# Performance work log

Hardware: AMD Instinct MI355X
Metric: run time of the kernel (lower is better)

## Reference

```python
import jax, jax.numpy as jnp
import numpy as np

EPS = 1e-6

def layer_norm(x, g, b):
    mu = jnp.mean(x, axis=-1, keepdims=True)
    var = jnp.mean((x - mu) ** 2, axis=-1, keepdims=True)
    return g * (x - mu) / jnp.sqrt(var + EPS) + b

def linear_mha(v_in, k_in, q_in, wq, bq, wk, bk, wv, bv, wo, bo, num_heads, d_model):
    b, s, _ = q_in.shape
    dv = d_model // num_heads
    q = q_in @ wq + bq                       # [b, s, h] (depth-1 per head)
    k = k_in @ wk + bk                       # [b, s, h]
    v = (v_in @ wv + bv).reshape(b, s, num_heads, dv).transpose(0, 2, 1, 3)  # [b,h,s,dv]
    q = q.transpose(0, 2, 1)                 # [b, h, s]
    k = k.transpose(0, 2, 1)                 # [b, h, s]
    # phi(k)^T v collapses seq: rank-1 per head -> [b, h, dv]
    kv = jnp.einsum('bhs,bhsd->bhd', jax.nn.sigmoid(k), v)
    # NOTE: tf.cumsum(axis=1) on shape (b, h, 1, dv) cumsums over the HEAD axis
    s_cum = jnp.cumsum(kv, axis=1)           # [b, h, dv]
    out = jnp.einsum('bhs,bhd->bhsd', jax.nn.sigmoid(q), s_cum)  # [b,h,s,dv]
    out = out.transpose(0, 2, 1, 3).reshape(b, s, d_model)
    return out @ wo + bo

def setup_inputs() -> dict:
    key = jax.random.key(0)
    ks = jax.random.split(key, 24)
    B, S, D, H, F = 4, 4096, 1024, 16, 4096
    gl = lambda k, shp: jax.random.uniform(k, shp, jnp.float32,
        -jnp.sqrt(6.0 / (shp[0] + shp[1])), jnp.sqrt(6.0 / (shp[0] + shp[1])))
    inp = {
        'x': jax.random.normal(ks[0], (B, S, D), jnp.float32),
        'enc': jax.random.normal(ks[1], (B, S, D), jnp.float32),
        'wq1': gl(ks[2], (D, H)), 'bq1': jnp.zeros((H,), jnp.float32),
        'wk1': gl(ks[3], (D, H)), 'bk1': jnp.zeros((H,), jnp.float32),
        'wv1': gl(ks[4], (D, D)), 'bv1': jnp.zeros((D,), jnp.float32),
        'wo1': gl(ks[5], (D, D)), 'bo1': jnp.zeros((D,), jnp.float32),
        'wq2': gl(ks[6], (D, H)), 'bq2': jnp.zeros((H,), jnp.float32),
        'wk2': gl(ks[7], (D, H)), 'bk2': jnp.zeros((H,), jnp.float32),
        'wv2': gl(ks[8], (D, D)), 'bv2': jnp.zeros((D,), jnp.float32),
        'wo2': gl(ks[9], (D, D)), 'bo2': jnp.zeros((D,), jnp.float32),
        'wf1': gl(ks[10], (D, F)), 'bf1': jnp.zeros((F,), jnp.float32),
        'wf2': gl(ks[11], (F, D)), 'bf2': jnp.zeros((D,), jnp.float32),
        'g1': jnp.ones((D,), jnp.float32), 'be1': jnp.zeros((D,), jnp.float32),
        'g2': jnp.ones((D,), jnp.float32), 'be2': jnp.zeros((D,), jnp.float32),
        'g3': jnp.ones((D,), jnp.float32), 'be3': jnp.zeros((D,), jnp.float32),
    }
    return inp

def reference(x, enc, wq1, bq1, wk1, bk1, wv1, bv1, wo1, bo1,
              wq2, bq2, wk2, bk2, wv2, bv2, wo2, bo2,
              wf1, bf1, wf2, bf2, g1, be1, g2, be2, g3, be3):
    H, D = 16, x.shape[-1]
    attn1 = linear_mha(x, x, x, wq1, bq1, wk1, bk1, wv1, bv1, wo1, bo1, H, D)
    out1 = layer_norm(attn1 + x, g1, be1)
    attn2 = linear_mha(enc, enc, out1, wq2, bq2, wk2, bk2, wv2, bv2, wo2, bo2, H, D)
    out2 = layer_norm(attn2 + out1, g2, be2)
    ffn = jax.nn.relu(out2 @ wf1 + bf1) @ wf2 + bf2
    out3 = layer_norm(ffn + out2, g3, be3)
    return (out3, jnp.zeros_like(out3), jnp.zeros_like(out3))
```

## Files before the change

### kernel.cpp

```cpp
#include <hip/hip_runtime.h>
#include <cstdint>

typedef unsigned short u16;
typedef __bf16 bf16x8 __attribute__((ext_vector_type(8)));
typedef float f32x4 __attribute__((ext_vector_type(4)));

__device__ __forceinline__ float bf2f(u16 h) {
  union { uint32_t u; float f; } v; v.u = (uint32_t)h << 16; return v.f;
}
__device__ __forceinline__ u16 f2bf(float f) {
  union { float f; uint32_t u; } v; v.f = f;
  uint32_t r = v.u + 0x7fffu + ((v.u >> 16) & 1u);
  return (u16)(r >> 16);
}
__device__ __forceinline__ float sigmoidf_(float x) {
  return 1.0f / (1.0f + __expf(-x));
}
__device__ __forceinline__ void load_lds16(const void* g, void* l) {
  __builtin_amdgcn_global_load_lds(
      (const __attribute__((address_space(1))) void*)g,
      (__attribute__((address_space(3))) void*)l, 16, 0, 0);
}
__device__ __forceinline__ bf16x8 cvt8(const float* p) {
  float4 a = *(const float4*)p, b = *(const float4*)(p + 4);
  union { u16 u[8]; bf16x8 v; } r;
  r.u[0] = f2bf(a.x); r.u[1] = f2bf(a.y); r.u[2] = f2bf(a.z); r.u[3] = f2bf(a.w);
  r.u[4] = f2bf(b.x); r.u[5] = f2bf(b.y); r.u[6] = f2bf(b.z); r.u[7] = f2bf(b.w);
  return r.v;
}
#define BAR() __builtin_amdgcn_s_barrier()

__global__ __launch_bounds__(256) void transpose_cvt(
    const float* __restrict__ in, u16* __restrict__ out, int K, int N) {
  __shared__ float t[32][33];
  int n0 = blockIdx.x * 32, k0 = blockIdx.y * 32;
  int tx = threadIdx.x & 31, ty = threadIdx.x >> 5;
#pragma unroll
  for (int i = 0; i < 32; i += 8)
    t[ty + i][tx] = in[(long)(k0 + ty + i) * N + n0 + tx];
  __syncthreads();
#pragma unroll
  for (int i = 0; i < 32; i += 8)
    out[(long)(n0 + ty + i) * K + k0 + tx] = f2bf(t[tx][ty + i]);
}

template <int QBF>
__global__ __launch_bounds__(256) void proj_mfma(
    const void* __restrict__ xq_, const float* __restrict__ xk,
    const float* __restrict__ wq, const float* __restrict__ bq,
    const float* __restrict__ wk, const float* __restrict__ bk,
    float* __restrict__ qout, float* __restrict__ kout) {
  __shared__ __attribute__((aligned(16))) u16 wt[2][16384];
  __shared__ __attribute__((aligned(16))) float red[4][64][8];
  const int tid = threadIdx.x;
  for (int kq = 0; kq < 4; kq++) {
    int k = kq * 256 + tid;
    const float4* q4 = (const float4*)(wq + (long)k * 16);
    const float4* k4 = (const float4*)(wk + (long)k * 16);
#pragma unroll
    for (int p = 0; p < 4; p++) {
      float4 qv = q4[p], kv = k4[p];
      float qf[4] = {qv.x, qv.y, qv.z, qv.w};
      float kf[4] = {kv.x, kv.y, kv.z, kv.w};
#pragma unroll
      for (int j = 0; j < 4; j++) {
        int c = p * 4 + j;
        int off = (c * 2048 + k * 2) ^ ((c & 7) << 4);
        *(u16*)((char*)wt[0] + off) = f2bf(qf[j]);
        *(u16*)((char*)wt[1] + off) = f2bf(kf[j]);
      }
    }
  }
  __syncthreads();
  const int wv = tid >> 6, lane = tid & 63;
  const int lrow = lane & 15, g = lane >> 4;
  const long tok0 = (long)blockIdx.x * 16;
  const long arow = (tok0 + lrow) * 1024 + wv * 256 + g * 8;
  const int swz = (lrow & 7) << 4;
  const int wbase = lrow * 2048 + wv * 512 + g * 16;
  f32x4 accq = {}, acck = {};
#pragma unroll
  for (int mf = 0; mf < 8; mf++) {
    bf16x8 aq_;
    if (QBF)
      aq_ = *(const bf16x8*)((const u16*)xq_ + arow + mf * 32);
    else
      aq_ = cvt8((const float*)xq_ + arow + mf * 32);
    bf16x8 ak_ = cvt8(xk + arow + mf * 32);
    int off = (wbase + mf * 64) ^ swz;
    bf16x8 bq_ = *(const bf16x8*)((const char*)wt[0] + off);
    bf16x8 bk_ = *(const bf16x8*)((const char*)wt[1] + off);
    accq = __builtin_amdgcn_mfma_f32_16x16x32_bf16(aq_, bq_, accq, 0, 0, 0);
    acck = __builtin_amdgcn_mfma_f32_16x16x32_bf16(ak_, bk_, acck, 0, 0, 0);
  }
  *(f32x4*)&red[wv][lane][0] = accq;
  *(f32x4*)&red[wv][lane][4] = acck;
  __syncthreads();
  if (tid < 64) {
    f32x4 q0 = *(const f32x4*)&red[0][tid][0];
    f32x4 k0 = *(const f32x4*)&red[0][tid][4];
#pragma unroll
    for (int w = 1; w < 4; w++) {
      q0 += *(const f32x4*)&red[w][tid][0];
      k0 += *(const f32x4*)&red[w][tid][4];
    }
    int col = tid & 15, r0 = (tid >> 4) * 4;
    float bqv = bq[col], bkv = bk[col];
#pragma unroll
    for (int i = 0; i < 4; i++) {
      qout[(tok0 + r0 + i) * 16 + col] = q0[i] + bqv;
      kout[(tok0 + r0 + i) * 16 + col] = k0[i] + bkv;
    }
  }
}

__global__ __launch_bounds__(256) void ksum(const float* __restrict__ kp,
                                            const float* __restrict__ x,
                                            float* __restrict__ ypart,
                                            float* __restrict__ spart) {
  __shared__ __attribute__((aligned(16))) float sk[256][20];
  __shared__ float ssl[16][17];
  const int tid = threadIdx.x;
  const int cc = blockIdx.x, sc = blockIdx.y, b = blockIdx.z;
  const int cl = tid & 63, sg = tid >> 6;
  const int col0 = cc * 128 + cl;
  float acc0[16], acc1[16];
#pragma unroll
  for (int h = 0; h < 16; h++) { acc0[h] = 0.f; acc1[h] = 0.f; }
  float ss = 0.f;
  for (int tile = 0; tile < 2; tile++) {
    const int s0 = sc * 512 + tile * 256;
    const float* kr = kp + ((long)b * 4096 + s0 + tid) * 16;
#pragma unroll
    for (int p = 0; p < 4; p++) {
      float4 k4 = *(const float4*)(kr + p * 4);
      *(float4*)&sk[tid][p * 4] = make_float4(
          sigmoidf_(k4.x), sigmoidf_(k4.y), sigmoidf_(k4.z), sigmoidf_(k4.w));
    }
    __syncthreads();
    {
      int g2 = tid >> 4, h2 = tid & 15;
      float s_ = 0.f;
#pragma unroll
      for (int i = 0; i < 16; i++) s_ += sk[g2 * 16 + i][h2];
      ssl[g2][h2] = s_;
    }
    __syncthreads();
    if (tid < 16) {
      float s_ = 0.f;
#pragma unroll
      for (int gg = 0; gg < 16; gg++) s_ += ssl[gg][tid];
      ss += s_;
    }
    const float* xr = x + ((long)b * 4096 + s0 + sg * 64) * 1024 + col0;
    for (int j = 0; j < 64; j++) {
      float xv0 = xr[(long)j * 1024];
      float xv1 = xr[(long)j * 1024 + 64];
      const float4* skr = (const float4*)sk[sg * 64 + j];
#pragma unroll
      for (int p = 0; p < 4; p++) {
        float4 s4 = skr[p];
        acc0[p * 4 + 0] += s4.x * xv0; acc1[p * 4 + 0] += s4.x * xv1;
        acc0[p * 4 + 1] += s4.y * xv0; acc1[p * 4 + 1] += s4.y * xv1;
        acc0[p * 4 + 2] += s4.z * xv0; acc1[p * 4 + 2] += s4.z * xv1;
        acc0[p * 4 + 3] += s4.w * xv0; acc1[p * 4 + 3] += s4.w * xv1;
      }
    }
    __syncthreads();
  }
  long pbase = (long)(b * 32 + sc * 4 + sg) * 16384 + col0;
#pragma unroll
  for (int h = 0; h < 16; h++) {
    ypart[pbase + h * 1024] = acc0[h];
    ypart[pbase + h * 1024 + 64] = acc1[h];
  }
  if (tid < 16) spart[(b * 8 + sc) * 16 + tid] = ss;
}

__global__ __launch_bounds__(256) void kv_small(
    const float* __restrict__ ypart, const float* __restrict__ spart,
    const float* __restrict__ wvw, const float* __restrict__ bv,
    float* __restrict__ kv) {
  __shared__ float yl[1024];
  __shared__ float red[4][64];
  const int tid = threadIdx.x;
  const int b = blockIdx.x >> 4, h = blockIdx.x & 15;
  for (int c = tid; c < 1024; c += 256) {
    float s_ = 0.f;
    const float* yp = ypart + (long)(b * 32) * 16384 + h * 1024 + c;
#pragma unroll
    for (int p = 0; p < 32; p++) s_ += yp[(long)p * 16384];
    yl[c] = s_;
  }
  __syncthreads();
  const int wv_ = tid >> 6, d = tid & 63;
  float acc = 0.f;
  const float* wcol = wvw + h * 64 + d;
  for (int c = wv_ * 256; c < wv_ * 256 + 256; c++)
    acc += yl[c] * wcol[(long)c * 1024];
  red[wv_][d] = acc;
  __syncthreads();
  if (tid < 64) {
    float ss = 0.f;
#pragma unroll
    for (int s_ = 0; s_ < 8; s_++) ss += spart[(b * 8 + s_) * 16 + h];
    kv[(b * 16 + h) * 64 + tid] = red[0][tid] + red[1][tid] + red[2][tid] +
                                  red[3][tid] + ss * bv[h * 64 + tid];
  }
}

__global__ __launch_bounds__(256) void zker(const float* __restrict__ kvb,
                                            const float* __restrict__ wo,
                                            float* __restrict__ z) {
  __shared__ float sc_[64];
  const int tid = threadIdx.x;
  const int b = blockIdx.x >> 4, h = blockIdx.x & 15;
  if (tid < 64) {
    float run = 0.f;
    for (int hh = 0; hh <= h; hh++) run += kvb[(b * 16 + hh) * 64 + tid];
    sc_[tid] = run;
  }
  __syncthreads();
  float4 acc = make_float4(0.f, 0.f, 0.f, 0.f);
  for (int d = 0; d < 64; d++) {
    float s_ = sc_[d];
    float4 w = ((const float4*)(wo + (long)(h * 64 + d) * 1024))[tid];
    acc.x += s_ * w.x; acc.y += s_ * w.y;
    acc.z += s_ * w.z; acc.w += s_ * w.w;
  }
  ((float4*)(z + (long)(b * 16 + h) * 1024))[tid] = acc;
}

template <int OMODE>
__global__ __launch_bounds__(256) void ln_attn(
    const float* __restrict__ qp, const float* __restrict__ z,
    const float* __restrict__ bo, const float* __restrict__ r,
    const float* __restrict__ g, const float* __restrict__ be,
    float* __restrict__ outf, u16* __restrict__ outb) {
  __shared__ float zs[16][1024];
  __shared__ float sq16[16];
  __shared__ float s1[4], s2[4];
  const int tid = threadIdx.x;
  const int b = blockIdx.x >> 8;
  const float4* zg = (const float4*)(z + (long)b * 16384);
  float4* zl = (float4*)zs;
#pragma unroll
  for (int i = 0; i < 16; i++) zl[i * 256 + tid] = zg[i * 256 + tid];
  float4 gv = ((const float4*)g)[tid];
  float4 bev = ((const float4*)be)[tid];
  float4 bov = ((const float4*)bo)[tid];
  const int wid = tid >> 6, lane = tid & 63;
  for (int rr_ = 0; rr_ < 16; rr_++) {
    long row = (long)blockIdx.x * 16 + rr_;
    if (tid < 16) sq16[tid] = sigmoidf_(qp[row * 16 + tid]);
    __syncthreads();
    float4 rv = ((const float4*)(r + row * 1024))[tid];
    float y0 = bov.x + rv.x, y1 = bov.y + rv.y;
    float y2 = bov.z + rv.z, y3 = bov.w + rv.w;
#pragma unroll
    for (int h = 0; h < 16; h++) {
      float s_ = sq16[h];
      float4 zv = *(const float4*)&zs[h][tid * 4];
      y0 += s_ * zv.x; y1 += s_ * zv.y; y2 += s_ * zv.z; y3 += s_ * zv.w;
    }
    float s = y0 + y1 + y2 + y3;
    float q = y0 * y0 + y1 * y1 + y2 * y2 + y3 * y3;
#pragma unroll
    for (int o = 32; o > 0; o >>= 1) {
      s += __shfl_down(s, o);
      q += __shfl_down(q, o);
    }
    if (lane == 0) { s1[wid] = s; s2[wid] = q; }
    __syncthreads();
    s = s1[0] + s1[1] + s1[2] + s1[3];
    q = s2[0] + s2[1] + s2[2] + s2[3];
    float mu = s * (1.f / 1024.f);
    float var = q * (1.f / 1024.f) - mu * mu;
    float inv = rsqrtf(fmaxf(var, 0.f) + 1e-6f);
    float o0 = gv.x * (y0 - mu) * inv + bev.x;
    float o1 = gv.y * (y1 - mu) * inv + bev.y;
    float o2 = gv.z * (y2 - mu) * inv + bev.z;
    float o3 = gv.w * (y3 - mu) * inv + bev.w;
    ((float4*)(outf + row * 1024))[tid] = make_float4(o0, o1, o2, o3);
    if (OMODE == 2) {
      uint2 ob;
      ob.x = (uint32_t)f2bf(o0) | ((uint32_t)f2bf(o1) << 16);
      ob.y = (uint32_t)f2bf(o2) | ((uint32_t)f2bf(o3) << 16);
      ((uint2*)(outb + row * 1024))[tid] = ob;
    }
    __syncthreads();
  }
}

template <int ACT>
__global__ __launch_bounds__(512) void gemm256(
    const u16* __restrict__ A, const u16* __restrict__ BT,
    const float* __restrict__ bias, u16* __restrict__ C, int M, int N,
    int K) {
  __shared__ __attribute__((aligned(16))) u16 lds[65536];
  const int tid = threadIdx.x;
  const int wid = tid >> 6, lane = tid & 63;
  const int wm = wid >> 2, wn = wid & 3;
  const int lrow = lane & 15, g = lane >> 4;

  int nwg = gridDim.x * gridDim.y;
  int orig = blockIdx.y * gridDim.x + blockIdx.x;
  int wg = (nwg & 7) ? orig : ((orig & 7) * (nwg >> 3) + (orig >> 3));
  const long bn = (long)(wg % gridDim.x) * 256;
  const long bm = (long)(wg / gridDim.x) * 256;

  const int rr = wid * 16 + (lane >> 2);
  const int esrc = ((lane & 3) * 8) ^ (((lane >> 5) & 1) * 16);
  const u16* Abase = A + (bm + rr) * (long)K + esrc;
  const u16* Bbase = BT + (bn + rr) * (long)K + esrc;
  const long jstep = (long)128 * K;
  char* ldsc = (char*)lds;
  const int ldsw = wid * 1024;

  const int swr = ((lrow >> 3) & 1) * 32;
  const int aoff = (wm * 128 + lrow) * 64 + ((g * 16) ^ swr);
  const int boff = 32768 + (wn * 64 + lrow) * 64 + ((g * 16) ^ swr);

  f32x4 acc[8][4] = {};
  const int KT = K >> 6;

  auto stage2 = [&](int buf, int kk, int kt, int half) {
    int dA = buf * 65536 + kk * 16384 + ldsw;
    if (half == 0) {
      const u16* sA = Abase + (long)kt * 64 + kk * 32;
      load_lds16(sA, ldsc + dA);
      load_lds16(sA + jstep, ldsc + dA + 8192);
    } else {
      const u16* sB = Bbase + (long)kt * 64 + kk * 32;
      load_lds16(sB, ldsc + dA + 32768);
      load_lds16(sB + jstep, ldsc + dA + 40960);
    }
  };

#define LDAB8(BUF, KK)                                                      \
  {                                                                         \
    const char* _b = ldsc + (BUF) * 65536 + (KK) * 16384;                   \
    _Pragma("unroll") for (int m = 0; m < 4; m++)                           \
        af[m] = *(const bf16x8*)(_b + aoff + m * 1024);                     \
    _Pragma("unroll") for (int n = 0; n < 4; n++)                           \
        bq[n] = *(const bf16x8*)(_b + boff + n * 1024);                     \
  }
#define LDA4(BUF, KK)                                                       \
  {                                                                         \
    const char* _b = ldsc + (BUF) * 65536 + (KK) * 16384;                   \
    _Pragma("unroll") for (int m = 4; m < 8; m++)                           \
        af[m] = *(const bf16x8*)(_b + aoff + m * 1024);                     \
  }
#define MMA16(M0)                                                           \
  __builtin_amdgcn_s_setprio(1);                                            \
  _Pragma("unroll") for (int m = M0; m < M0 + 4; m++)                       \
  _Pragma("unroll") for (int n = 0; n < 4; n++)                             \
      acc[m][n] = __builtin_amdgcn_mfma_f32_16x16x32_bf16(af[m], bq[n],     \
                                                          acc[m][n], 0, 0,  \
                                                          0);               \
  __builtin_amdgcn_s_setprio(0);
#define WLG0() asm volatile("s_waitcnt lgkmcnt(0)" ::: "memory")
#define WVM4() asm volatile("s_waitcnt vmcnt(4)" ::: "memory")
#define WVM0() asm volatile("s_waitcnt vmcnt(0)" ::: "memory")

  bf16x8 af[8], bq[4];

  stage2(0, 0, 0, 0);
  stage2(0, 0, 0, 1);
  stage2(0, 1, 0, 0);
  stage2(0, 1, 0, 1);
  WVM4();
  BAR();

  for (int kt = 0; kt + 1 < KT; ++kt) {
    const int b0 = kt & 1, b1 = b0 ^ 1;
    LDAB8(b0, 0);
    stage2(b1, 0, kt + 1, 0);
    BAR(); WLG0();
    MMA16(0);
    BAR();
    LDA4(b0, 0);
    stage2(b1, 0, kt + 1, 1);
    WVM4();
    BAR(); WLG0();
    MMA16(4);
    BAR();
    LDAB8(b0, 1);
    stage2(b1, 1, kt + 1, 0);
    BAR(); WLG0();
    MMA16(0);
    BAR();
    LDA4(b0, 1);
    stage2(b1, 1, kt + 1, 1);
    WVM4();
    BAR(); WLG0();
    MMA16(4);
    BAR();
  }
  {
    const int b0 = (KT - 1) & 1;
    LDAB8(b0, 0);
    BAR(); WLG0();
    MMA16(0);
    BAR();
    LDA4(b0, 0);
    WVM0();
    BAR(); WLG0();
    MMA16(4);
    BAR();
    LDAB8(b0, 1);
    BAR(); WLG0();
    MMA16(0);
    BAR();
    LDA4(b0, 1);
    BAR(); WLG0();
    MMA16(4);
    BAR();
  }

#pragma unroll
  for (int n = 0; n < 4; n++) {
    int cl = wn * 64 + n * 16 + lrow;
    float bb = bias[bn + cl];
#pragma unroll
    for (int m = 0; m < 8; m++) {
      int rl = wm * 128 + m * 16 + g * 4;
#pragma unroll
      for (int i = 0; i < 4; i++) {
        float v = acc[m][n][i] + bb;
        if (ACT == 1) v = fmaxf(v, 0.f);
        lds[(rl + i) * 256 + cl] = f2bf(v);
      }
    }
  }
  BAR();
  const uint4* lv = (const uint4*)lds;
#pragma unroll
  for (int it = 0; it < 16; it++) {
    int idx = it * 512 + tid;
    int row = idx >> 5;
    int cu = (idx & 31) * 8;
    *(uint4*)&C[(bm + row) * (long)N + bn + cu] = lv[idx];
  }
#undef LDAB8
#undef LDA4
#undef MMA16
#undef WLG0
#undef WVM4
#undef WVM0
}

__global__ __launch_bounds__(256) void ln_res(const u16* __restrict__ a,
                                              const float* __restrict__ r,
                                              const float* __restrict__ g,
                                              const float* __restrict__ be,
                                              float* __restrict__ outf) {
  long row = blockIdx.x;
  int tid = threadIdx.x;
  uint2 av = ((const uint2*)(a + row * 1024))[tid];
  float4 rv = ((const float4*)(r + row * 1024))[tid];
  float y[4];
  y[0] = bf2f((u16)(av.x & 0xffff)) + rv.x;
  y[1] = bf2f((u16)(av.x >> 16)) + rv.y;
  y[2] = bf2f((u16)(av.y & 0xffff)) + rv.z;
  y[3] = bf2f((u16)(av.y >> 16)) + rv.w;
  float s = y[0] + y[1] + y[2] + y[3];
  float q = y[0] * y[0] + y[1] * y[1] + y[2] * y[2] + y[3] * y[3];
#pragma unroll
  for (int o = 32; o > 0; o >>= 1) {
    s += __shfl_down(s, o);
    q += __shfl_down(q, o);
  }
  __shared__ float s1[4], s2[4];
  int wid = tid >> 6, lane = tid & 63;
  if (lane == 0) { s1[wid] = s; s2[wid] = q; }
  __syncthreads();
  s = s1[0] + s1[1] + s1[2] + s1[3];
  q = s2[0] + s2[1] + s2[2] + s2[3];
  float mu = s * (1.f / 1024.f);
  float var = q * (1.f / 1024.f) - mu * mu;
  float inv = rsqrtf(fmaxf(var, 0.f) + 1e-6f);
  float4 gv = ((const float4*)g)[tid], bv = ((const float4*)be)[tid];
  float o0 = gv.x * (y[0] - mu) * inv + bv.x;
  float o1 = gv.y * (y[1] - mu) * inv + bv.y;
  float o2 = gv.z * (y[2] - mu) * inv + bv.z;
  float o3 = gv.w * (y[3] - mu) * inv + bv.w;
  ((float4*)(outf + row * 1024))[tid] = make_float4(o0, o1, o2, o3);
}

extern "C" void kernel_launch(void* const* d_in, const int* in_sizes, int n_in,
                              void* d_out, int out_size, void* d_ws,
                              size_t ws_size, hipStream_t stream) {
  const float* x   = (const float*)d_in[0];
  const float* enc = (const float*)d_in[1];
  const float* wq1 = (const float*)d_in[2];  const float* bq1 = (const float*)d_in[3];
  const float* wk1 = (const float*)d_in[4];  const float* bk1 = (const float*)d_in[5];
  const float* wv1 = (const float*)d_in[6];  const float* bv1 = (const float*)d_in[7];
  const float* wo1 = (const float*)d_in[8];  const float* bo1 = (const float*)d_in[9];
  const float* wq2 = (const float*)d_in[10]; const float* bq2 = (const float*)d_in[11];
  const float* wk2 = (const float*)d_in[12]; const float* bk2 = (const float*)d_in[13];
  const float* wv2 = (const float*)d_in[14]; const float* bv2 = (const float*)d_in[15];
  const float* wo2 = (const float*)d_in[16]; const float* bo2 = (const float*)d_in[17];
  const float* wf1 = (const float*)d_in[18]; const float* bf1 = (const float*)d_in[19];
  const float* wf2 = (const float*)d_in[20]; const float* bf2 = (const float*)d_in[21];
  const float* g1 = (const float*)d_in[22];  const float* be1 = (const float*)d_in[23];
  const float* g2 = (const float*)d_in[24];  const float* be2 = (const float*)d_in[25];
  const float* g3 = (const float*)d_in[26];  const float* be3 = (const float*)d_in[27];
  (void)in_sizes; (void)n_in; (void)out_size; (void)ws_size;

  const size_t S = (size_t)16384 * 1024;
  float* O0 = (float*)d_out;

  char* base = (char*)d_ws;
  size_t off = 0;
  auto alloc = [&](size_t bytes) -> void* {
    void* p = base + off;
    off += (bytes + 255) & ~(size_t)255;
    return p;
  };
  u16* WT1    = (u16*)alloc((size_t)4096 * 1024 * 2);
  u16* WT2    = (u16*)alloc((size_t)4096 * 1024 * 2);
  float* qb   = (float*)alloc((size_t)16384 * 16 * 4);
  float* kb   = (float*)alloc((size_t)16384 * 16 * 4);
  float* ypart= (float*)alloc((size_t)4 * 32 * 16 * 1024 * 4);
  float* spart= (float*)alloc((size_t)4 * 8 * 16 * 4);
  float* kvb  = (float*)alloc((size_t)4 * 16 * 64 * 4);
  float* zb   = (float*)alloc((size_t)4 * 16 * 1024 * 4);
  u16* FA     = (u16*)alloc(S * 2);
  u16* FM     = (u16*)alloc((size_t)16384 * 4096 * 2);
  u16* O1b    = (u16*)alloc(S * 2);
  u16* O2b    = (u16*)alloc(S * 2);
  float* O1f  = (float*)alloc(S * 4);
  float* O2f  = (float*)alloc(S * 4);

  const int T = 16384;
  dim3 blk(256), gblk(512);

  proj_mfma<0><<<1024, blk, 0, stream>>>(x, x, wq1, bq1, wk1, bk1, qb, kb);
  ksum<<<dim3(8, 8, 4), blk, 0, stream>>>(kb, x, ypart, spart);
  kv_small<<<64, blk, 0, stream>>>(ypart, spart, wv1, bv1, kvb);
  zker<<<64, blk, 0, stream>>>(kvb, wo1, zb);
  ln_attn<2><<<1024, blk, 0, stream>>>(qb, zb, bo1, x, g1, be1, O1f, O1b);

  proj_mfma<1><<<1024, blk, 0, stream>>>(O1b, enc, wq2, bq2, wk2, bk2, qb, kb);
  ksum<<<dim3(8, 8, 4), blk, 0, stream>>>(kb, enc, ypart, spart);
  kv_small<<<64, blk, 0, stream>>>(ypart, spart, wv2, bv2, kvb);
  zker<<<64, blk, 0, stream>>>(kvb, wo2, zb);
  ln_attn<2><<<1024, blk, 0, stream>>>(qb, zb, bo2, O1f, g2, be2, O2f, O2b);

  transpose_cvt<<<dim3(128, 32), blk, 0, stream>>>(wf1, WT1, 1024, 4096);
  transpose_cvt<<<dim3(32, 128), blk, 0, stream>>>(wf2, WT2, 4096, 1024);
  gemm256<1><<<dim3(16, 64), gblk, 0, stream>>>(O2b, WT1, bf1, FM, T, 4096, 1024);
  gemm256<0><<<dim3(4, 64), gblk, 0, stream>>>(FM, WT2, bf2, FA, T, 1024, 4096);
  ln_res<<<16384, blk, 0, stream>>>(FA, O2f, g3, be3, O0);

  hipMemsetAsync((float*)d_out + S, 0, 2 * S * 4, stream);
}
```

Before: 593.2 us.

## Give each wave its own token tile in q/k projection, drop LDS reduction

The q/k projection kernel now assigns each wave a full 16-token row tile over the whole K dimension instead of splitting K across four waves. This removes the LDS cross-wave reduction and its barrier, and cuts the grid from 1024 to 256 blocks, so each block's per-block conversion of the weights into LDS is amortised over four times as many tokens. For the first layer, where q and k share the same input, a SAME template flag reuses the converted A fragment instead of loading and converting x twice. The cost is fewer blocks (less parallelism) and a longer serial MFMA chain per wave.

```diff
diff --git a/kernel.cpp b/kernel.cpp
--- a/kernel.cpp
+++ b/kernel.cpp
@@ -44,14 +44,13 @@
     out[(long)(n0 + ty + i) * K + k0 + tx] = f2bf(t[tx][ty + i]);
 }
 
-template <int QBF>
+template <int SAME, int QBF>
 __global__ __launch_bounds__(256) void proj_mfma(
     const void* __restrict__ xq_, const float* __restrict__ xk,
     const float* __restrict__ wq, const float* __restrict__ bq,
     const float* __restrict__ wk, const float* __restrict__ bk,
     float* __restrict__ qout, float* __restrict__ kout) {
   __shared__ __attribute__((aligned(16))) u16 wt[2][16384];
-  __shared__ __attribute__((aligned(16))) float red[4][64][8];
   const int tid = threadIdx.x;
   for (int kq = 0; kq < 4; kq++) {
     int k = kq * 256 + tid;
@@ -74,43 +73,34 @@
   __syncthreads();
   const int wv = tid >> 6, lane = tid & 63;
   const int lrow = lane & 15, g = lane >> 4;
-  const long tok0 = (long)blockIdx.x * 16;
-  const long arow = (tok0 + lrow) * 1024 + wv * 256 + g * 8;
+  const long tok0 = (long)blockIdx.x * 64 + wv * 16;
   const int swz = (lrow & 7) << 4;
-  const int wbase = lrow * 2048 + wv * 512 + g * 16;
+  const long arow = (tok0 + lrow) * 1024 + g * 8;
   f32x4 accq = {}, acck = {};
-#pragma unroll
-  for (int mf = 0; mf < 8; mf++) {
+#pragma unroll 8
+  for (int ks = 0; ks < 32; ks++) {
     bf16x8 aq_;
     if (QBF)
-      aq_ = *(const bf16x8*)((const u16*)xq_ + arow + mf * 32);
+      aq_ = *(const bf16x8*)((const u16*)xq_ + arow + ks * 32);
     else
-      aq_ = cvt8((const float*)xq_ + arow + mf * 32);
-    bf16x8 ak_ = cvt8(xk + arow + mf * 32);
-    int off = (wbase + mf * 64) ^ swz;
+      aq_ = cvt8((const float*)xq_ + arow + ks * 32);
+    bf16x8 ak_;
+    if (SAME)
+      ak_ = aq_;
+    else
+      ak_ = cvt8(xk + arow + ks * 32);
+    int off = (lrow * 2048 + ks * 64 + g * 16) ^ swz;
     bf16x8 bq_ = *(const bf16x8*)((const char*)wt[0] + off);
     bf16x8 bk_ = *(const bf16x8*)((const char*)wt[1] + off);
     accq = __builtin_amdgcn_mfma_f32_16x16x32_bf16(aq_, bq_, accq, 0, 0, 0);
     acck = __builtin_amdgcn_mfma_f32_16x16x32_bf16(ak_, bk_, acck, 0, 0, 0);
   }
-  *(f32x4*)&red[wv][lane][0] = accq;
-  *(f32x4*)&red[wv][lane][4] = acck;
-  __syncthreads();
-  if (tid < 64) {
-    f32x4 q0 = *(const f32x4*)&red[0][tid][0];
-    f32x4 k0 = *(const f32x4*)&red[0][tid][4];
-#pragma unroll
-    for (int w = 1; w < 4; w++) {
-      q0 += *(const f32x4*)&red[w][tid][0];
-      k0 += *(const f32x4*)&red[w][tid][4];
-    }
-    int col = tid & 15, r0 = (tid >> 4) * 4;
-    float bqv = bq[col], bkv = bk[col];
-#pragma unroll
-    for (int i = 0; i < 4; i++) {
-      qout[(tok0 + r0 + i) * 16 + col] = q0[i] + bqv;
-      kout[(tok0 + r0 + i) * 16 + col] = k0[i] + bkv;
-    }
+  const int col = lrow, r0 = g * 4;
+  float bqv = bq[col], bkv = bk[col];
+#pragma unroll
+  for (int i = 0; i < 4; i++) {
+    qout[(tok0 + r0 + i) * 16 + col] = accq[i] + bqv;
+    kout[(tok0 + r0 + i) * 16 + col] = acck[i] + bkv;
   }
 }
 
@@ -536,13 +526,15 @@
   const int T = 16384;
   dim3 blk(256), gblk(512);
 
-  proj_mfma<0><<<1024, blk, 0, stream>>>(x, x, wq1, bq1, wk1, bk1, qb, kb);
+  proj_mfma<1, 0><<<256, blk, 0, stream>>>(x, nullptr, wq1, bq1, wk1, bk1,
+                                           qb, kb);
   ksum<<<dim3(8, 8, 4), blk, 0, stream>>>(kb, x, ypart, spart);
   kv_small<<<64, blk, 0, stream>>>(ypart, spart, wv1, bv1, kvb);
   zker<<<64, blk, 0, stream>>>(kvb, wo1, zb);
   ln_attn<2><<<1024, blk, 0, stream>>>(qb, zb, bo1, x, g1, be1, O1f, O1b);
 
-  proj_mfma<1><<<1024, blk, 0, stream>>>(O1b, enc, wq2, bq2, wk2, bk2, qb, kb);
+  proj_mfma<0, 1><<<256, blk, 0, stream>>>(O1b, enc, wq2, bq2, wk2, bk2,
+                                           qb, kb);
   ksum<<<dim3(8, 8, 4), blk, 0, stream>>>(kb, enc, ypart, spart);
   kv_small<<<64, blk, 0, stream>>>(ypart, spart, wv2, bv2, kvb);
   zker<<<64, blk, 0, stream>>>(kvb, wo2, zb);
```

Result: no change. 593.1 us (-0.0%).
